# Optimization experiments

Measured on AMD Instinct MI355X. Metric: run time of the kernel, lower is better.

## Reference

```python
import jax, jax.numpy as jnp
import numpy as np

B, N = 512, 128
NFEAT, NHID, NHEADS, HID = 133, 60, 8, 300
FP_DIM, FP2, TASK = 1489, 512, 1
ALPHA = 0.2
NEG = -9e15


def _lin(k, fi, fo):
    s = 1.0 / np.sqrt(fi)
    return jax.random.uniform(k, (fi, fo), minval=-s, maxval=s, dtype=jnp.float32)


def _vec(k, fi, n):
    s = 1.0 / np.sqrt(fi)
    return jax.random.uniform(k, (n,), minval=-s, maxval=s, dtype=jnp.float32)


def setup_inputs() -> dict:
    key = jax.random.key(0)
    ks = jax.random.split(key, 24)
    x = jax.random.normal(ks[0], (B, N, NFEAT), dtype=jnp.float32)
    adj = jax.random.randint(ks[1], (B, N, N), 0, 2, dtype=jnp.int32)
    adj = jnp.maximum(adj, jnp.eye(N, dtype=jnp.int32)[None])  # ensure valid softmax rows
    fp = jax.random.uniform(ks[2], (B, FP_DIM), dtype=jnp.float32)
    # multi-head GAT params (W has no bias; attention vector a split into src/dst halves)
    sW = 1.0 / np.sqrt(NFEAT)
    W_heads = jax.random.uniform(ks[3], (NHEADS, NFEAT, NHID), minval=-sW, maxval=sW, dtype=jnp.float32)
    sa = 1.0 / np.sqrt(2 * NHID)
    a_src = jax.random.uniform(ks[4], (NHEADS, NHID), minval=-sa, maxval=sa, dtype=jnp.float32)
    a_dst = jax.random.uniform(ks[5], (NHEADS, NHID), minval=-sa, maxval=sa, dtype=jnp.float32)
    W_out = _lin(ks[6], NHEADS * NHID, HID)
    ao_src = _vec(ks[7], 2 * HID, HID)
    ao_dst = _vec(ks[8], 2 * HID, HID)
    fc1_w = _lin(ks[9], FP_DIM, FP2); fc1_b = _vec(ks[10], FP_DIM, FP2)
    fc2_w = _lin(ks[11], FP2, HID); fc2_b = _vec(ks[12], FP2, HID)
    fcg_w = _lin(ks[13], HID, HID); fcg_b = _vec(ks[14], HID, HID)
    fcf_w = _lin(ks[15], HID, HID); fcf_b = _vec(ks[16], HID, HID)
    ffn1_w = _lin(ks[17], 2 * HID, HID); ffn1_b = _vec(ks[18], 2 * HID, HID)
    ffn2_w = _lin(ks[19], HID, TASK); ffn2_b = _vec(ks[20], HID, TASK)
    return {"x": x, "adj": adj, "fp": fp, "W_heads": W_heads, "a_src": a_src,
            "a_dst": a_dst, "W_out": W_out, "ao_src": ao_src, "ao_dst": ao_dst,
            "fc1_w": fc1_w, "fc1_b": fc1_b, "fc2_w": fc2_w, "fc2_b": fc2_b,
            "fcg_w": fcg_w, "fcg_b": fcg_b, "fcf_w": fcf_w, "fcf_b": fcf_b,
            "ffn1_w": ffn1_w, "ffn1_b": ffn1_b, "ffn2_w": ffn2_w, "ffn2_b": ffn2_b}


def reference(x, adj, fp, W_heads, a_src, a_dst, W_out, ao_src, ao_dst,
              fc1_w, fc1_b, fc2_w, fc2_b, fcg_w, fcg_b, fcf_w, fcf_b,
              ffn1_w, ffn1_b, ffn2_w, ffn2_b):
    adjm = adj > 0  # [B,N,N]
    # --- multi-head GAT layer (dropout = identity in eval) ---
    Wh = jnp.einsum('bnf,hfo->bhno', x, W_heads)              # [B,H,N,nhid]
    s = jnp.einsum('bhno,ho->bhn', Wh, a_src)
    d = jnp.einsum('bhno,ho->bhn', Wh, a_dst)
    # e_ij = leakyrelu(a . [Wh_i ; Wh_j]) without materializing [N,N,2F]
    e = jax.nn.leaky_relu(s[:, :, :, None] + d[:, :, None, :], ALPHA)
    e = jnp.where(adjm[:, None], e, NEG)
    att = jax.nn.softmax(e, axis=-1)                          # softmax over neighbors j
    hp = jax.nn.elu(jnp.einsum('bhnm,bhmo->bhno', att, Wh))   # concat=True head output
    h = hp.transpose(0, 2, 1, 3).reshape(B, N, NHEADS * NHID)
    # --- output GAT layer (concat=False) ---
    Wo = h @ W_out                                            # [B,N,HID]
    eo = jax.nn.leaky_relu((Wo @ ao_src)[:, :, None] + (Wo @ ao_dst)[:, None, :], ALPHA)
    eo = jnp.where(adjm, eo, NEG)
    ho = jax.nn.softmax(eo, axis=-1) @ Wo
    ho = jax.nn.log_softmax(jax.nn.elu(ho), axis=-1)          # log_softmax over features (dim=1 in torch)
    gat = ho.mean(axis=1)                                     # sum over atoms / atom_size
    # --- FPN branch ---
    f = jax.nn.relu(fp @ fc1_w + fc1_b)
    f = f @ fc2_w + fc2_b
    # --- fusion (gat_scale = 0.5) ---
    g = jax.nn.relu(gat @ fcg_w + fcg_b)
    f = jax.nn.relu(f @ fcf_w + fcf_b)
    z = jnp.concatenate([g, f], axis=1)                       # [B, 2*HID]
    z = jax.nn.relu(z @ ffn1_w + ffn1_b)
    z = z @ ffn2_w + ffn2_b
    return jax.nn.sigmoid(z)                                  # is_classif, eval mode
```

## Files before the change

kernel.cpp:

```cpp
#include <hip/hip_runtime.h>
#include <hip/hip_bf16.h>
#include <math.h>
#include <stdint.h>

#define LRA 0.2f

typedef __attribute__((ext_vector_type(8))) short bf16x8;
typedef __attribute__((ext_vector_type(8))) unsigned short u16x8;
typedef __attribute__((ext_vector_type(4))) float f32x4;
typedef unsigned long long u64;

__device__ __forceinline__ unsigned short f2bf(float v) {
  union { __hip_bfloat16 b; unsigned short u; } c;
  c.b = __float2bfloat16(v);
  return c.u;
}
__device__ __forceinline__ float bf2f(unsigned short h) {
  union { float f; unsigned int u; } a; a.u = ((unsigned int)h) << 16;
  return a.f;
}
__device__ __forceinline__ float warp_sum(float v){
  #pragma unroll
  for (int s = 32; s; s >>= 1) v += __shfl_xor(v, s);
  return v;
}

__global__ __launch_bounds__(256) void k_mask(const int* __restrict__ adj, u64* __restrict__ mg){
  const int t = threadIdx.x, lane = t & 63, w = t >> 6, b = blockIdx.x;
  const int* adjb = adj + (size_t)b * 128 * 128;
  for (int i = w * 32; i < w * 32 + 32; ++i) {
    u64 b0 = __ballot(adjb[i * 128 + lane] > 0);
    u64 b1 = __ballot(adjb[i * 128 + 64 + lane] > 0);
    if (lane == 0) { mg[((size_t)b * 128 + i) * 2] = b0; mg[((size_t)b * 128 + i) * 2 + 1] = b1; }
  }
}

__global__ __launch_bounds__(64) void k_prep1(
    const float* __restrict__ Whw, unsigned short* __restrict__ BH, unsigned short* __restrict__ BL)
{
  const int kt = blockIdx.x, nt = blockIdx.y, l = threadIdx.x;
  const int n = nt * 16 + (l & 15), k0 = kt * 32 + (l >> 4) * 8;
  const int hd = n / 60, j = n - hd * 60;
  uint4 hv, lv;
  unsigned int* hp = (unsigned int*)&hv;
  unsigned int* lp = (unsigned int*)&lv;
  #pragma unroll
  for (int p = 0; p < 4; ++p) {
    unsigned short hh[2], ll[2];
    #pragma unroll
    for (int e = 0; e < 2; ++e) {
      const int k = k0 + p * 2 + e;
      const float v = (n < 480 && k < 133) ? Whw[((size_t)hd * 133 + k) * 60 + j] : 0.f;
      const unsigned short h = f2bf(v);
      hh[e] = h; ll[e] = f2bf(v - bf2f(h));
    }
    hp[p] = hh[0] | ((unsigned int)hh[1] << 16);
    lp[p] = ll[0] | ((unsigned int)ll[1] << 16);
  }
  const size_t off = (((size_t)(kt * 32 + nt)) * 64 + l) * 8;
  *(uint4*)&BH[off] = hv;
  *(uint4*)&BL[off] = lv;
}

__global__ __launch_bounds__(64) void k_prep2(
    const float* __restrict__ W, unsigned short* __restrict__ BH, unsigned short* __restrict__ BL)
{
  const int kt = blockIdx.x, nt = blockIdx.y, l = threadIdx.x;
  const int n = nt * 16 + (l & 15), k0 = kt * 32 + (l >> 4) * 8;
  uint4 hv, lv;
  unsigned int* hp = (unsigned int*)&hv;
  unsigned int* lp = (unsigned int*)&lv;
  #pragma unroll
  for (int p = 0; p < 4; ++p) {
    unsigned short hh[2], ll[2];
    #pragma unroll
    for (int e = 0; e < 2; ++e) {
      const int k = k0 + p * 2 + e;
      const float v = (n < 300 && k < 480) ? W[(size_t)k * 300 + n] : 0.f;
      const unsigned short h = f2bf(v);
      hh[e] = h; ll[e] = f2bf(v - bf2f(h));
    }
    hp[p] = hh[0] | ((unsigned int)hh[1] << 16);
    lp[p] = ll[0] | ((unsigned int)ll[1] << 16);
  }
  const size_t off = (((size_t)(kt * 20 + nt)) * 64 + l) * 8;
  *(uint4*)&BH[off] = hv;
  *(uint4*)&BL[off] = lv;
}

__global__ __launch_bounds__(512) void k_gemm1(
    const float* __restrict__ x,
    const unsigned short* __restrict__ BH, const unsigned short* __restrict__ BL,
    const float* __restrict__ asrc, const float* __restrict__ adst,
    unsigned int* __restrict__ buf1, float* __restrict__ s1g, float* __restrict__ d1g)
{
  __shared__ unsigned int Apk[64][32];
  __shared__ float asl[512], adl[512];
  __shared__ float sp0[8][64], sp1[8][64], dp0[8][64], dp1[8][64];
  const int t = threadIdx.x, lane = t & 63, w = t >> 6, r = lane & 15, g = lane >> 4;
  const int b = blockIdx.x >> 1, p = blockIdx.x & 1;
  const int row0 = p * 64;
  const float* xb = x + (size_t)b * 128 * 133;
  unsigned int* slab = buf1 + (size_t)b * 61440;

  asl[t] = (t < 480) ? asrc[t] : 0.f;
  adl[t] = (t < 480) ? adst[t] : 0.f;

  f32x4 acc[4][4];
  #pragma unroll
  for (int mt = 0; mt < 4; ++mt)
    #pragma unroll
    for (int ntl = 0; ntl < 4; ++ntl) acc[mt][ntl] = (f32x4){0.f,0.f,0.f,0.f};

  for (int kt = 0; kt < 5; ++kt) {
    {
      const int row_l = t >> 3, sl = t & 7;
      const int k0 = kt * 32 + sl * 4;
      uint4 pk;
      unsigned int* pp = (unsigned int*)&pk;
      #pragma unroll
      for (int e = 0; e < 4; ++e) {
        const int k = k0 + e;
        const float v = (k < 133) ? xb[(size_t)(row0 + row_l) * 133 + k] : 0.f;
        const unsigned short h = f2bf(v);
        pp[e] = ((unsigned int)h << 16) | f2bf(v - bf2f(h));
      }
      *(uint4*)&Apk[row_l][((sl ^ (row_l & 7)) << 2)] = pk;
    }
    bf16x8 bh[4], bl[4];
    #pragma unroll
    for (int ntl = 0; ntl < 4; ++ntl) {
      const int nt = w * 4 + ntl;
      const size_t off = (((size_t)(kt * 32 + nt)) * 64 + lane) * 8;
      bh[ntl] = *(const bf16x8*)&BH[off];
      bl[ntl] = *(const bf16x8*)&BL[off];
    }
    __syncthreads();
    #pragma unroll
    for (int mt = 0; mt < 4; ++mt) {
      const int row_l = mt * 16 + r, key = r & 7;
      const uint4 p0 = *(const uint4*)&Apk[row_l][(((2*g)   ^ key) << 2)];
      const uint4 p1 = *(const uint4*)&Apk[row_l][(((2*g+1) ^ key) << 2)];
      const unsigned int pw[8] = {p0.x,p0.y,p0.z,p0.w,p1.x,p1.y,p1.z,p1.w};
      bf16x8 ah, al;
      #pragma unroll
      for (int e = 0; e < 8; ++e) { ah[e] = (short)(pw[e] >> 16); al[e] = (short)(pw[e] & 0xffffu); }
      #pragma unroll
      for (int ntl = 0; ntl < 4; ++ntl) {
        acc[mt][ntl] = __builtin_amdgcn_mfma_f32_16x16x32_bf16(ah, bh[ntl], acc[mt][ntl], 0,0,0);
        acc[mt][ntl] = __builtin_amdgcn_mfma_f32_16x16x32_bf16(al, bh[ntl], acc[mt][ntl], 0,0,0);
        acc[mt][ntl] = __builtin_amdgcn_mfma_f32_16x16x32_bf16(ah, bl[ntl], acc[mt][ntl], 0,0,0);
      }
    }
    __syncthreads();
  }
  #pragma unroll
  for (int mt = 0; mt < 4; ++mt)
    #pragma unroll
    for (int ntl = 0; ntl < 4; ++ntl) {
      const int cc = (w * 4 + ntl) * 16 + r;
      if (cc < 480) {
        const int hd = cc / 60, cl = cc - hd * 60;
        uint4 pv;
        unsigned int* pp = (unsigned int*)&pv;
        #pragma unroll
        for (int q = 0; q < 4; ++q) {
          const float v = acc[mt][ntl][q];
          const unsigned short h = f2bf(v);
          pp[q] = ((unsigned int)h << 16) | f2bf(v - bf2f(h));
        }
        *(uint4*)&slab[(size_t)hd * 7680 + (size_t)cl * 128 + row0 + mt * 16 + (g << 2)] = pv;
      }
    }
  const int thr0 = 60 - 4 * w;
  #pragma unroll
  for (int mt = 0; mt < 4; ++mt) {
    #pragma unroll
    for (int q = 0; q < 4; ++q) {
      float s0 = 0.f, s1 = 0.f, d0 = 0.f, d1 = 0.f;
      #pragma unroll
      for (int ntl = 0; ntl < 4; ++ntl) {
        const int loc = ntl * 16 + r;
        const int cc = w * 64 + loc;
        const float a = acc[mt][ntl][q];
        const float as = asl[cc], ad = adl[cc];
        if (loc < thr0) { s0 += a * as; d0 += a * ad; }
        else            { s1 += a * as; d1 += a * ad; }
      }
      #pragma unroll
      for (int s = 1; s <= 8; s <<= 1) {
        s0 += __shfl_xor(s0, s); s1 += __shfl_xor(s1, s);
        d0 += __shfl_xor(d0, s); d1 += __shfl_xor(d1, s);
      }
      if (r == 0) {
        const int row_l = mt * 16 + g * 4 + q;
        sp0[w][row_l] = s0; sp1[w][row_l] = s1;
        dp0[w][row_l] = d0; dp1[w][row_l] = d1;
      }
    }
  }
  __syncthreads();
  {
    const int hd = t >> 6, row_l = t & 63;
    s1g[((size_t)b * 8 + hd) * 128 + row0 + row_l] = sp0[hd][row_l] + (hd > 0 ? sp1[hd-1][row_l] : 0.f);
    d1g[((size_t)b * 8 + hd) * 128 + row0 + row_l] = dp0[hd][row_l] + (hd > 0 ? dp1[hd-1][row_l] : 0.f);
  }
}

__device__ __forceinline__ float make_att_frags(
    const float si, const u64 ma, const u64 mb2, const float* darr,
    const int g, bf16x8* pah, bf16x8* pal)
{
  const unsigned int mby[4] = {
    (unsigned int)(ma  >> (g * 8)) & 0xffu,
    (unsigned int)(ma  >> (32 + g * 8)) & 0xffu,
    (unsigned int)(mb2 >> (g * 8)) & 0xffu,
    (unsigned int)(mb2 >> (32 + g * 8)) & 0xffu };
  float ev[4][8];
  float mx = -3e38f;
  #pragma unroll
  for (int kt = 0; kt < 4; ++kt)
    #pragma unroll
    for (int e = 0; e < 8; ++e) {
      const int j = ((kt & 1) * 32) + ((kt >> 1) * 64) + g * 8 + e;
      float v = si + darr[j];
      v = fmaxf(v, LRA * v);
      const float vv = (mby[((kt & 1) << 1) | (kt >> 1)] & (1u << e)) ? v : -3e38f;
      ev[kt][e] = vv;
      mx = fmaxf(mx, vv);
    }
  mx = fmaxf(mx, __shfl_xor(mx, 16));
  mx = fmaxf(mx, __shfl_xor(mx, 32));
  float sum = 0.f;
  #pragma unroll
  for (int kt = 0; kt < 4; ++kt)
    #pragma unroll
    for (int e = 0; e < 8; ++e) {
      const float p = (ev[kt][e] > -1e37f) ? __expf(ev[kt][e] - mx) : 0.f;
      ev[kt][e] = p;
      sum += p;
    }
  sum += __shfl_xor(sum, 16);
  sum += __shfl_xor(sum, 32);
  #pragma unroll
  for (int kt = 0; kt < 4; ++kt) {
    const int ks = ((kt & 1) << 1) | (kt >> 1);
    union { unsigned int u[4]; bf16x8 v; } hw, lw;
    #pragma unroll
    for (int p2 = 0; p2 < 4; ++p2) {
      const float p0 = ev[ks][2 * p2], p1 = ev[ks][2 * p2 + 1];
      const unsigned short h0 = f2bf(p0), h1 = f2bf(p1);
      hw.u[p2] = h0 | ((unsigned int)h1 << 16);
      lw.u[p2] = f2bf(p0 - bf2f(h0)) | ((unsigned int)f2bf(p1 - bf2f(h1)) << 16);
    }
    pah[kt] = hw.v;
    pal[kt] = lw.v;
  }
  return 1.f / sum;
}

__global__ __launch_bounds__(256) void k_att1(
    unsigned int* __restrict__ buf1, const u64* __restrict__ mg,
    const float* __restrict__ s1g, const float* __restrict__ d1g)
{
  __shared__ unsigned short Th[16][64][8], Tl[16][64][8];
  __shared__ float sarr[128], darr[128];
  __shared__ u64 mAr[128], mBr[128];
  const int t = threadIdx.x, lane = t & 63, w = t >> 6, r = lane & 15, g = lane >> 4;
  const int bid = blockIdx.x;
  const int lb = ((bid & 7) << 9) | (bid >> 3);
  const int b = lb >> 3, hd = lb & 7;
  const size_t sl = (size_t)b * 8 + hd;
  unsigned int* slab = buf1 + sl * 7680;

  if (t < 128) {
    sarr[t] = s1g[sl * 128 + t];
    darr[t] = d1g[sl * 128 + t];
    mAr[t] = mg[((size_t)b * 128 + t) * 2];
    mBr[t] = mg[((size_t)b * 128 + t) * 2 + 1];
  }
  #pragma unroll
  for (int ii = 0; ii < 4; ++ii) {
    const int idx = t + ii * 256;
    const int c = idx & 63, jg = idx >> 6;
    uint4 p0 = {0,0,0,0}, p1 = {0,0,0,0};
    if (c < 60) {
      const uint4* src = (const uint4*)&slab[(size_t)c * 128 + jg * 8];
      p0 = src[0]; p1 = src[1];
    }
    const unsigned int pw[8] = {p0.x,p0.y,p0.z,p0.w,p1.x,p1.y,p1.z,p1.w};
    u16x8 hv, lv;
    #pragma unroll
    for (int e = 0; e < 8; ++e) { hv[e] = (unsigned short)(pw[e] >> 16); lv[e] = (unsigned short)(pw[e] & 0xffffu); }
    const int tile = ((c >> 4) << 2) | (jg >> 2);
    const int li = ((jg & 3) << 4) | (c & 15);
    *(u16x8*)&Th[tile][li][0] = hv;
    *(u16x8*)&Tl[tile][li][0] = lv;
  }
  __syncthreads();
  bf16x8 pah[2][4], pal[2][4];
  float inv2[2];
  #pragma unroll
  for (int mt = 0; mt < 2; ++mt) {
    const int i = w * 32 + mt * 16 + r;
    inv2[mt] = make_att_frags(sarr[i], mAr[i], mBr[i], darr, g, pah[mt], pal[mt]);
  }
  f32x4 acc[2][4];
  #pragma unroll
  for (int mt = 0; mt < 2; ++mt)
    #pragma unroll
    for (int nt = 0; nt < 4; ++nt) acc[mt][nt] = (f32x4){0.f,0.f,0.f,0.f};
  #pragma unroll
  for (int kt = 0; kt < 4; ++kt)
    #pragma unroll
    for (int nt = 0; nt < 4; ++nt) {
      const bf16x8 bh = *(const bf16x8*)&Th[(nt << 2) | kt][lane][0];
      const bf16x8 bl = *(const bf16x8*)&Tl[(nt << 2) | kt][lane][0];
      #pragma unroll
      for (int mt = 0; mt < 2; ++mt) {
        acc[mt][nt] = __builtin_amdgcn_mfma_f32_16x16x32_bf16(pah[mt][kt], bh, acc[mt][nt], 0,0,0);
        acc[mt][nt] = __builtin_amdgcn_mfma_f32_16x16x32_bf16(pal[mt][kt], bh, acc[mt][nt], 0,0,0);
        acc[mt][nt] = __builtin_amdgcn_mfma_f32_16x16x32_bf16(pah[mt][kt], bl, acc[mt][nt], 0,0,0);
      }
    }
  #pragma unroll
  for (int mt = 0; mt < 2; ++mt) {
    float sc[4];
    #pragma unroll
    for (int q = 0; q < 4; ++q) sc[q] = __shfl(inv2[mt], g * 4 + q);
    #pragma unroll
    for (int nt = 0; nt < 4; ++nt) {
      const int cc = nt * 16 + r;
      if (cc < 60) {
        #pragma unroll
        for (int q = 0; q < 4; ++q) {
          const int row = w * 32 + mt * 16 + g * 4 + q;
          float v = acc[mt][nt][q] * sc[q];
          v = v > 0.f ? v : __expf(v) - 1.f;
          const unsigned short h = f2bf(v), l = f2bf(v - bf2f(h));
          slab[(size_t)row * 60 + cc] = ((unsigned int)h << 16) | l;
        }
      }
    }
  }
}

__global__ __launch_bounds__(256, 3) void k_gemm2(
    unsigned int* __restrict__ buf1,
    const unsigned short* __restrict__ BH, const unsigned short* __restrict__ BL,
    const float* __restrict__ aos, const float* __restrict__ aod,
    float* __restrict__ s2g, float* __restrict__ d2g)
{
  __shared__ unsigned int Apk[64][32];
  __shared__ float aosl[320], aodl[320];
  __shared__ float sred[4][64], dred[4][64];
  const int t = threadIdx.x, lane = t & 63, w = t >> 6, r = lane & 15, g = lane >> 4;
  const int b = blockIdx.x >> 1, p = blockIdx.x & 1;
  const int row0 = p * 64;
  unsigned int* slab = buf1 + (size_t)b * 61440;
  if (t < 320) { aosl[t] = t < 300 ? aos[t] : 0.f; aodl[t] = t < 300 ? aod[t] : 0.f; }

  f32x4 acc[4][5];
  #pragma unroll
  for (int mt = 0; mt < 4; ++mt)
    #pragma unroll
    for (int ntl = 0; ntl < 5; ++ntl) acc[mt][ntl] = (f32x4){0.f,0.f,0.f,0.f};

  for (int kt = 0; kt < 15; ++kt) {
    #pragma unroll
    for (int i = 0; i < 2; ++i) {
      const int idx = t + i * 256, row_l = idx >> 3, sl = idx & 7;
      const int k0 = kt * 32 + sl * 4;
      const int hd = k0 / 60, c = k0 - hd * 60;
      const uint4 v = *(const uint4*)&slab[(size_t)hd * 7680 + (size_t)(row0 + row_l) * 60 + c];
      *(uint4*)&Apk[row_l][((sl ^ (row_l & 7)) << 2)] = v;
    }
    bf16x8 bh[5], bl[5];
    #pragma unroll
    for (int ntl = 0; ntl < 5; ++ntl) {
      const int nt = w * 5 + ntl;
      const size_t off = (((size_t)(kt * 20 + nt)) * 64 + lane) * 8;
      bh[ntl] = *(const bf16x8*)&BH[off];
      bl[ntl] = *(const bf16x8*)&BL[off];
    }
    __syncthreads();
    #pragma unroll
    for (int mt = 0; mt < 4; ++mt) {
      const int row_l = mt * 16 + r, key = r & 7;
      const uint4 p0 = *(const uint4*)&Apk[row_l][(((2*g)   ^ key) << 2)];
      const uint4 p1 = *(const uint4*)&Apk[row_l][(((2*g+1) ^ key) << 2)];
      const unsigned int pw[8] = {p0.x,p0.y,p0.z,p0.w,p1.x,p1.y,p1.z,p1.w};
      bf16x8 ah, al;
      #pragma unroll
      for (int e = 0; e < 8; ++e) { ah[e] = (short)(pw[e] >> 16); al[e] = (short)(pw[e] & 0xffffu); }
      #pragma unroll
      for (int ntl = 0; ntl < 5; ++ntl) {
        acc[mt][ntl] = __builtin_amdgcn_mfma_f32_16x16x32_bf16(ah, bh[ntl], acc[mt][ntl], 0,0,0);
        acc[mt][ntl] = __builtin_amdgcn_mfma_f32_16x16x32_bf16(al, bh[ntl], acc[mt][ntl], 0,0,0);
        acc[mt][ntl] = __builtin_amdgcn_mfma_f32_16x16x32_bf16(ah, bl[ntl], acc[mt][ntl], 0,0,0);
      }
    }
    __syncthreads();
  }
  #pragma unroll
  for (int mt = 0; mt < 4; ++mt)
    #pragma unroll
    for (int ntl = 0; ntl < 5; ++ntl) {
      const int cc = w * 80 + ntl * 16 + r;
      if (cc < 300) {
        uint4 pv;
        unsigned int* pp = (unsigned int*)&pv;
        #pragma unroll
        for (int q = 0; q < 4; ++q) {
          const float v = acc[mt][ntl][q];
          const unsigned short h = f2bf(v);
          pp[q] = ((unsigned int)h << 16) | f2bf(v - bf2f(h));
        }
        *(uint4*)&slab[(size_t)cc * 128 + row0 + mt * 16 + (g << 2)] = pv;
      }
    }
  #pragma unroll
  for (int mt = 0; mt < 4; ++mt) {
    #pragma unroll
    for (int q = 0; q < 4; ++q) {
      float sv = 0.f, dv = 0.f;
      #pragma unroll
      for (int ntl = 0; ntl < 5; ++ntl) {
        const int cc = w * 80 + ntl * 16 + r;
        const float a = acc[mt][ntl][q];
        sv += a * aosl[cc]; dv += a * aodl[cc];
      }
      #pragma unroll
      for (int s = 1; s <= 8; s <<= 1) { sv += __shfl_xor(sv, s); dv += __shfl_xor(dv, s); }
      if (r == 0) {
        const int row_l = mt * 16 + g * 4 + q;
        sred[w][row_l] = sv; dred[w][row_l] = dv;
      }
    }
  }
  __syncthreads();
  if (t < 64) {
    s2g[(size_t)b * 128 + row0 + t] = sred[0][t] + sred[1][t] + sred[2][t] + sred[3][t];
    d2g[(size_t)b * 128 + row0 + t] = dred[0][t] + dred[1][t] + dred[2][t] + dred[3][t];
  }
}

__global__ __launch_bounds__(256) void k_att2(
    const unsigned int* __restrict__ buf1, const u64* __restrict__ mg,
    const float* __restrict__ s2g, const float* __restrict__ d2g,
    float* __restrict__ gat)
{
  __shared__ unsigned short Th[16][64][8], Tl[16][64][8];
  __shared__ float sarr[128], darr[128];
  __shared__ u64 mAr[128], mBr[128];
  __shared__ float colsum[304];
  __shared__ float srow[16];
  const int t = threadIdx.x, lane = t & 63, w = t >> 6, r = lane & 15, g = lane >> 4;
  const int b = blockIdx.x;
  const unsigned int* slab = buf1 + (size_t)b * 61440;

  if (t < 128) {
    sarr[t] = s2g[(size_t)b * 128 + t];
    darr[t] = d2g[(size_t)b * 128 + t];
    mAr[t] = mg[((size_t)b * 128 + t) * 2];
    mBr[t] = mg[((size_t)b * 128 + t) * 2 + 1];
  }
  for (int c = t; c < 304; c += 256) colsum[c] = 0.f;
  __syncthreads();
  bf16x8 pah[2][4], pal[2][4];
  float inv2[2];
  #pragma unroll
  for (int mt = 0; mt < 2; ++mt) {
    const int i = w * 32 + mt * 16 + r;
    inv2[mt] = make_att_frags(sarr[i], mAr[i], mBr[i], darr, g, pah[mt], pal[mt]);
  }
  float scq[2][4];
  #pragma unroll
  for (int mt = 0; mt < 2; ++mt)
    #pragma unroll
    for (int q = 0; q < 4; ++q) scq[mt][q] = __shfl(inv2[mt], g * 4 + q);

  float m8[2][4], l8[2][4];
  #pragma unroll
  for (int mt = 0; mt < 2; ++mt)
    #pragma unroll
    for (int q = 0; q < 4; ++q) { m8[mt][q] = -3e38f; l8[mt][q] = 0.f; }

  for (int ch = 0; ch < 5; ++ch) {
    #pragma unroll
    for (int ii = 0; ii < 4; ++ii) {
      const int idx = t + ii * 256;
      const int c = idx & 63, jg = idx >> 6;
      const int gc = ch * 64 + c;
      uint4 p0 = {0,0,0,0}, p1 = {0,0,0,0};
      if (gc < 300) {
        const uint4* src = (const uint4*)&slab[(size_t)gc * 128 + jg * 8];
        p0 = src[0]; p1 = src[1];
      }
      const unsigned int pw[8] = {p0.x,p0.y,p0.z,p0.w,p1.x,p1.y,p1.z,p1.w};
      u16x8 hv, lv;
      #pragma unroll
      for (int e = 0; e < 8; ++e) { hv[e] = (unsigned short)(pw[e] >> 16); lv[e] = (unsigned short)(pw[e] & 0xffffu); }
      const int tile = ((c >> 4) << 2) | (jg >> 2);
      const int li = ((jg & 3) << 4) | (c & 15);
      *(u16x8*)&Th[tile][li][0] = hv;
      *(u16x8*)&Tl[tile][li][0] = lv;
    }
    __syncthreads();
    f32x4 pacc[2][4];
    #pragma unroll
    for (int mt = 0; mt < 2; ++mt)
      #pragma unroll
      for (int nt = 0; nt < 4; ++nt) pacc[mt][nt] = (f32x4){0.f,0.f,0.f,0.f};
    #pragma unroll
    for (int kt = 0; kt < 4; ++kt)
      #pragma unroll
      for (int nt = 0; nt < 4; ++nt) {
        const bf16x8 bh = *(const bf16x8*)&Th[(nt << 2) | kt][lane][0];
        const bf16x8 bl = *(const bf16x8*)&Tl[(nt << 2) | kt][lane][0];
        #pragma unroll
        for (int mt = 0; mt < 2; ++mt) {
          pacc[mt][nt] = __builtin_amdgcn_mfma_f32_16x16x32_bf16(pah[mt][kt], bh, pacc[mt][nt], 0,0,0);
          pacc[mt][nt] = __builtin_amdgcn_mfma_f32_16x16x32_bf16(pal[mt][kt], bh, pacc[mt][nt], 0,0,0);
          pacc[mt][nt] = __builtin_amdgcn_mfma_f32_16x16x32_bf16(pah[mt][kt], bl, pacc[mt][nt], 0,0,0);
        }
      }
    float csA[4] = {0,0,0,0};
    #pragma unroll
    for (int mt = 0; mt < 2; ++mt) {
      float vq[4][4];
      #pragma unroll
      for (int nt = 0; nt < 4; ++nt) {
        const int cc = ch * 64 + nt * 16 + r;
        const bool cv = cc < 300;
        #pragma unroll
        for (int q = 0; q < 4; ++q) {
          float v = pacc[mt][nt][q] * scq[mt][q];
          v = v > 0.f ? v : __expf(v) - 1.f;
          vq[nt][q] = cv ? v : -3e38f;
          csA[nt] += cv ? v : 0.f;
        }
      }
      #pragma unroll
      for (int q = 0; q < 4; ++q) {
        float mx = fmaxf(fmaxf(vq[0][q], vq[1][q]), fmaxf(vq[2][q], vq[3][q]));
        mx = fmaxf(mx, __shfl_xor(mx, 1));
        mx = fmaxf(mx, __shfl_xor(mx, 2));
        mx = fmaxf(mx, __shfl_xor(mx, 4));
        mx = fmaxf(mx, __shfl_xor(mx, 8));
        const float nm = fmaxf(m8[mt][q], mx);
        float ps = __expf(vq[0][q]-nm) + __expf(vq[1][q]-nm) + __expf(vq[2][q]-nm) + __expf(vq[3][q]-nm);
        ps += __shfl_xor(ps, 1); ps += __shfl_xor(ps, 2);
        ps += __shfl_xor(ps, 4); ps += __shfl_xor(ps, 8);
        l8[mt][q] = l8[mt][q] * __expf(m8[mt][q] - nm) + ps;
        m8[mt][q] = nm;
      }
    }
    #pragma unroll
    for (int nt = 0; nt < 4; ++nt) {
      float cs = csA[nt];
      cs += __shfl_xor(cs, 16); cs += __shfl_xor(cs, 32);
      const int cc = ch * 64 + nt * 16 + r;
      if (g == 0 && cc < 300) atomicAdd(&colsum[cc], cs);
    }
    __syncthreads();
  }
  if (r == 0) {
    float sp = 0.f;
    #pragma unroll
    for (int mt = 0; mt < 2; ++mt)
      #pragma unroll
      for (int q = 0; q < 4; ++q) sp += m8[mt][q] + __logf(l8[mt][q]);
    srow[w * 4 + g] = sp;
  }
  __syncthreads();
  float S = 0.f;
  #pragma unroll
  for (int k = 0; k < 16; ++k) S += srow[k];
  for (int c = t; c < 300; c += 256)
    gat[(size_t)b * 300 + c] = (colsum[c] - S) * (1.f / 128.f);
}

__global__ __launch_bounds__(256) void k_gemm_sk(
    const float* __restrict__ A, const float* __restrict__ B,
    float* __restrict__ P, int M, int K, int N, int kpt)
{
  __shared__ unsigned short Ah[64][40], Al[64][40], Bh[64][40], Bl[64][40];
  const int t = threadIdx.x, lane = t & 63, w = t >> 6, r = lane & 15, g = lane >> 4;
  const int row0 = blockIdx.x * 64, col0 = blockIdx.y * 64;
// ... 30 lines not shown
      unsigned short h0 = f2bf(v0), h1 = f2bf(v1);
      *(unsigned int*)&Bh[n][kk] = h0 | ((unsigned int)h1 << 16);
      unsigned short l0 = f2bf(v0 - bf2f(h0)), l1 = f2bf(v1 - bf2f(h1));
      *(unsigned int*)&Bl[n][kk] = l0 | ((unsigned int)l1 << 16);
    }
    __syncthreads();
    const bf16x8 ah  = *(const bf16x8*)&Ah[w * 16 + r][g * 8];
    const bf16x8 al2 = *(const bf16x8*)&Al[w * 16 + r][g * 8];
    #pragma unroll
    for (int nt = 0; nt < 4; ++nt) {
      const bf16x8 bh = *(const bf16x8*)&Bh[nt * 16 + r][g * 8];
      const bf16x8 bl = *(const bf16x8*)&Bl[nt * 16 + r][g * 8];
      acc[nt] = __builtin_amdgcn_mfma_f32_16x16x32_bf16(ah,  bh, acc[nt], 0,0,0);
      acc[nt] = __builtin_amdgcn_mfma_f32_16x16x32_bf16(al2, bh, acc[nt], 0,0,0);
      acc[nt] = __builtin_amdgcn_mfma_f32_16x16x32_bf16(ah,  bl, acc[nt], 0,0,0);
    }
    __syncthreads();
  }
  float* Pout = P + (size_t)sk * M * N;
  #pragma unroll
  for (int nt = 0; nt < 4; ++nt) {
    const int cc = col0 + nt * 16 + r;
    if (cc < N) {
      #pragma unroll
      for (int q = 0; q < 4; ++q)
        Pout[(size_t)(row0 + w * 16 + g * 4 + q) * N + cc] = acc[nt][q];
    }
  }
}

__global__ __launch_bounds__(256) void k_reduce(
    const float* __restrict__ P, const float* __restrict__ bias,
    float* __restrict__ C, int M, int N, int ldc, int nsk, int act)
{
  const int idx = blockIdx.x * 256 + threadIdx.x;
  if (idx >= M * N) return;
  const int row = idx / N, col = idx - row * N;
  float s = bias[col];
  for (int k = 0; k < nsk; ++k) s += P[(size_t)k * M * N + idx];
  if (act) s = fmaxf(s, 0.f);
  C[(size_t)row * ldc + col] = s;
}

__global__ __launch_bounds__(512) void k_out(
    const float* __restrict__ z1, const float* __restrict__ w2,
    const float* __restrict__ b2, float* __restrict__ out)
{
  const int t = threadIdx.x, lane = t & 63, w = t >> 6;
  const int b = blockIdx.x * 8 + w;
  float p = 0.f;
  for (int k = lane; k < 300; k += 64) p += z1[(size_t)b * 300 + k] * w2[k];
  p = warp_sum(p);
  if (lane == 0) out[b] = 1.f / (1.f + __expf(-(p + b2[0])));
}

extern "C" void kernel_launch(void* const* d_in, const int* in_sizes, int n_in,
                              void* d_out, int out_size, void* d_ws, size_t ws_size,
                              hipStream_t stream)
{
  const float* x    = (const float*)d_in[0];
  const int*   adj  = (const int*)d_in[1];
  const float* fp   = (const float*)d_in[2];
  const float* Whw  = (const float*)d_in[3];
  const float* asrc = (const float*)d_in[4];
  const float* adst = (const float*)d_in[5];
  const float* Wout = (const float*)d_in[6];
  const float* aos  = (const float*)d_in[7];
  const float* aod  = (const float*)d_in[8];
  const float* fc1w = (const float*)d_in[9];
  const float* fc1b = (const float*)d_in[10];
  const float* fc2w = (const float*)d_in[11];
  const float* fc2b = (const float*)d_in[12];
  const float* fcgw = (const float*)d_in[13];
  const float* fcgb = (const float*)d_in[14];
  const float* fcfw = (const float*)d_in[15];
  const float* fcfb = (const float*)d_in[16];
  const float* f1w  = (const float*)d_in[17];
  const float* f1b  = (const float*)d_in[18];
  const float* f2w  = (const float*)d_in[19];
  const float* f2b  = (const float*)d_in[20];
  float* out = (float*)d_out;

  char* wsb = (char*)d_ws;
  unsigned int* buf1 = (unsigned int*)wsb;
  float* s1g = (float*)(wsb + 125829120);
  float* d1g = (float*)(wsb + 127926272);
  float* s2g = (float*)(wsb + 130023424);
  float* d2g = (float*)(wsb + 130285568);
  u64*   mgb = (u64*)  (wsb + 130547712);
  float* gatp = (float*)(wsb + 131596288);
  float* fpnp = (float*)(wsb + 132210688);
  float* f1buf = (float*)(wsb + 132825088);
  float* zb    = (float*)(wsb + 133873664);
  float* z1b   = (float*)(wsb + 135102464);
  float* P0 = (float*)(wsb + 135716864);
  float* P1 = (float*)(wsb + 142008320);
  float* P2 = (float*)(wsb + 144465920);
  float* P3 = (float*)(wsb + 145694720);
  float* P4 = (float*)(wsb + 146923520);
  unsigned short* Bf1H = (unsigned short*)(wsb + 149381120);
  unsigned short* Bf1L = (unsigned short*)(wsb + 149544960);
  unsigned short* Bf2H = (unsigned short*)(wsb + 149708800);
  unsigned short* Bf2L = (unsigned short*)(wsb + 150016000);

  k_prep1<<<dim3(5, 32), 64, 0, stream>>>(Whw, Bf1H, Bf1L);
  k_prep2<<<dim3(15, 20), 64, 0, stream>>>(Wout, Bf2H, Bf2L);
  k_mask <<<512, 256, 0, stream>>>(adj, mgb);
  k_gemm1<<<1024, 512, 0, stream>>>(x, Bf1H, Bf1L, asrc, adst, buf1, s1g, d1g);
  k_att1 <<<4096, 256, 0, stream>>>(buf1, mgb, s1g, d1g);
  k_gemm2<<<1024, 256, 0, stream>>>(buf1, Bf2H, Bf2L, aos, aod, s2g, d2g);
  k_att2 <<<512, 256, 0, stream>>>(buf1, mgb, s2g, d2g, gatp);
  k_gemm_sk<<<dim3(8,8,6), 256, 0, stream>>>(fp, fc1w, P0, 512, 1489, 512, 8);
  k_reduce<<<1024, 256, 0, stream>>>(P0, fc1b, f1buf, 512, 512, 512, 6, 1);
  k_gemm_sk<<<dim3(8,5,4), 256, 0, stream>>>(f1buf, fc2w, P1, 512, 512, 300, 4);
  k_reduce<<<600, 256, 0, stream>>>(P1, fc2b, fpnp, 512, 300, 300, 4, 0);
  k_gemm_sk<<<dim3(8,5,2), 256, 0, stream>>>(gatp, fcgw, P2, 512, 300, 300, 5);
  k_gemm_sk<<<dim3(8,5,2), 256, 0, stream>>>(fpnp, fcfw, P3, 512, 300, 300, 5);
  k_reduce<<<600, 256, 0, stream>>>(P2, fcgb, zb, 512, 300, 600, 2, 1);
  k_reduce<<<600, 256, 0, stream>>>(P3, fcfb, zb + 300, 512, 300, 600, 2, 1);
  k_gemm_sk<<<dim3(8,5,4), 256, 0, stream>>>(zb, f1w, P4, 512, 600, 300, 5);
  k_reduce<<<600, 256, 0, stream>>>(P4, f1b, z1b, 512, 300, 300, 4, 1);
  k_out<<<64, 512, 0, stream>>>(z1b, f2w, f2b, out);
}
```

Baseline: 376.6 us.

## Split attention score projections out of GEMM kernels into separate kernels

Removes the fused src/dst attention-score epilogues from k_gemm1 and k_gemm2 and computes them in new lightweight kernels (k_sd1, k_sd2) that reread the stored hi/lo bf16 outputs from global memory. k_gemm1 also halves its row tile from 64 to 32 rows, doubling the grid, and only half the threads stage A. The aim is to cut register and shared-memory pressure in the GEMMs and raise occupancy. In exchange it adds two kernel launches and an extra pass over the intermediate buffers. The scores are now computed from the split-rounded stored values rather than the fp32 accumulators.

After: 383.8 us. About the same (+1.9%).

```diff
diff --git a/kernel.cpp b/kernel.cpp
--- a/kernel.cpp
+++ b/kernel.cpp
@@ -91,29 +91,23 @@
 __global__ __launch_bounds__(512) void k_gemm1(
     const float* __restrict__ x,
     const unsigned short* __restrict__ BH, const unsigned short* __restrict__ BL,
-    const float* __restrict__ asrc, const float* __restrict__ adst,
-    unsigned int* __restrict__ buf1, float* __restrict__ s1g, float* __restrict__ d1g)
-{
-  __shared__ unsigned int Apk[64][32];
-  __shared__ float asl[512], adl[512];
-  __shared__ float sp0[8][64], sp1[8][64], dp0[8][64], dp1[8][64];
+    unsigned int* __restrict__ buf1)
+{
+  __shared__ unsigned int Apk[32][32];
   const int t = threadIdx.x, lane = t & 63, w = t >> 6, r = lane & 15, g = lane >> 4;
-  const int b = blockIdx.x >> 1, p = blockIdx.x & 1;
-  const int row0 = p * 64;
+  const int b = blockIdx.x >> 2, p = blockIdx.x & 3;
+  const int row0 = p * 32;
   const float* xb = x + (size_t)b * 128 * 133;
   unsigned int* slab = buf1 + (size_t)b * 61440;
 
-  asl[t] = (t < 480) ? asrc[t] : 0.f;
-  adl[t] = (t < 480) ? adst[t] : 0.f;
-
-  f32x4 acc[4][4];
-  #pragma unroll
-  for (int mt = 0; mt < 4; ++mt)
+  f32x4 acc[2][4];
+  #pragma unroll
+  for (int mt = 0; mt < 2; ++mt)
     #pragma unroll
     for (int ntl = 0; ntl < 4; ++ntl) acc[mt][ntl] = (f32x4){0.f,0.f,0.f,0.f};
 
   for (int kt = 0; kt < 5; ++kt) {
-    {
+    if (t < 256) {
       const int row_l = t >> 3, sl = t & 7;
       const int k0 = kt * 32 + sl * 4;
       uint4 pk;
@@ -137,7 +131,7 @@
     }
     __syncthreads();
     #pragma unroll
-    for (int mt = 0; mt < 4; ++mt) {
+    for (int mt = 0; mt < 2; ++mt) {
       const int row_l = mt * 16 + r, key = r & 7;
       const uint4 p0 = *(const uint4*)&Apk[row_l][(((2*g)   ^ key) << 2)];
       const uint4 p1 = *(const uint4*)&Apk[row_l][(((2*g+1) ^ key) << 2)];
@@ -155,7 +149,7 @@
     __syncthreads();
   }
   #pragma unroll
-  for (int mt = 0; mt < 4; ++mt)
+  for (int mt = 0; mt < 2; ++mt)
     #pragma unroll
     for (int ntl = 0; ntl < 4; ++ntl) {
       const int cc = (w * 4 + ntl) * 16 + r;
@@ -172,39 +166,45 @@
         *(uint4*)&slab[(size_t)hd * 7680 + (size_t)cl * 128 + row0 + mt * 16 + (g << 2)] = pv;
       }
     }
-  const int thr0 = 60 - 4 * w;
-  #pragma unroll
-  for (int mt = 0; mt < 4; ++mt) {
-    #pragma unroll
-    for (int q = 0; q < 4; ++q) {
-      float s0 = 0.f, s1 = 0.f, d0 = 0.f, d1 = 0.f;
-      #pragma unroll
-      for (int ntl = 0; ntl < 4; ++ntl) {
-        const int loc = ntl * 16 + r;
-        const int cc = w * 64 + loc;
-        const float a = acc[mt][ntl][q];
-        const float as = asl[cc], ad = adl[cc];
-        if (loc < thr0) { s0 += a * as; d0 += a * ad; }
-        else            { s1 += a * as; d1 += a * ad; }
-      }
-      #pragma unroll
-      for (int s = 1; s <= 8; s <<= 1) {
-        s0 += __shfl_xor(s0, s); s1 += __shfl_xor(s1, s);
-        d0 += __shfl_xor(d0, s); d1 += __shfl_xor(d1, s);
-      }
-      if (r == 0) {
-        const int row_l = mt * 16 + g * 4 + q;
-        sp0[w][row_l] = s0; sp1[w][row_l] = s1;
-        dp0[w][row_l] = d0; dp1[w][row_l] = d1;
-      }
-    }
-  }
-  __syncthreads();
-  {
-    const int hd = t >> 6, row_l = t & 63;
-    s1g[((size_t)b * 8 + hd) * 128 + row0 + row_l] = sp0[hd][row_l] + (hd > 0 ? sp1[hd-1][row_l] : 0.f);
-    d1g[((size_t)b * 8 + hd) * 128 + row0 + row_l] = dp0[hd][row_l] + (hd > 0 ? dp1[hd-1][row_l] : 0.f);
-  }
+}
+
+__global__ __launch_bounds__(64) void k_sd1(
+    const unsigned int* __restrict__ buf1, const float* __restrict__ asrc,
+    const float* __restrict__ adst, float* __restrict__ s1g, float* __restrict__ d1g)
+{
+  const int lane = threadIdx.x, sl = blockIdx.x, hd = sl & 7;
+  const unsigned int* slab = buf1 + (size_t)sl * 7680;
+  float s0 = 0.f, s1v = 0.f, d0 = 0.f, d1v = 0.f;
+  #pragma unroll 4
+  for (int c = 0; c < 60; ++c) {
+    const float ac = asrc[hd * 60 + c], dc = adst[hd * 60 + c];
+    const unsigned int p0 = slab[c * 128 + lane];
+    const unsigned int p1 = slab[c * 128 + 64 + lane];
+    const float v0 = bf2f((unsigned short)(p0 >> 16)) + bf2f((unsigned short)(p0 & 0xffffu));
+    const float v1 = bf2f((unsigned short)(p1 >> 16)) + bf2f((unsigned short)(p1 & 0xffffu));
+    s0 += v0 * ac; d0 += v0 * dc;
+    s1v += v1 * ac; d1v += v1 * dc;
+  }
+  s1g[(size_t)sl * 128 + lane] = s0;      d1g[(size_t)sl * 128 + lane] = d0;
+  s1g[(size_t)sl * 128 + 64 + lane] = s1v; d1g[(size_t)sl * 128 + 64 + lane] = d1v;
+}
+
+__global__ __launch_bounds__(128) void k_sd2(
+    const unsigned int* __restrict__ buf1, const float* __restrict__ aos,
+    const float* __restrict__ aod, float* __restrict__ s2g, float* __restrict__ d2g)
+{
+  const int j = threadIdx.x, b = blockIdx.x;
+  const unsigned int* slab = buf1 + (size_t)b * 61440;
+  float s = 0.f, d = 0.f;
+  #pragma unroll 4
+  for (int c = 0; c < 300; ++c) {
+    const float ac = aos[c], dc = aod[c];
+    const unsigned int pk = slab[(size_t)c * 128 + j];
+    const float v = bf2f((unsigned short)(pk >> 16)) + bf2f((unsigned short)(pk & 0xffffu));
+    s += v * ac; d += v * dc;
+  }
+  s2g[(size_t)b * 128 + j] = s;
+  d2g[(size_t)b * 128 + j] = d;
 }
 
 __device__ __forceinline__ float make_att_frags(
@@ -347,18 +347,13 @@
 
 __global__ __launch_bounds__(256, 3) void k_gemm2(
     unsigned int* __restrict__ buf1,
-    const unsigned short* __restrict__ BH, const unsigned short* __restrict__ BL,
-    const float* __restrict__ aos, const float* __restrict__ aod,
-    float* __restrict__ s2g, float* __restrict__ d2g)
+    const unsigned short* __restrict__ BH, const unsigned short* __restrict__ BL)
 {
   __shared__ unsigned int Apk[64][32];
-  __shared__ float aosl[320], aodl[320];
-  __shared__ float sred[4][64], dred[4][64];
   const int t = threadIdx.x, lane = t & 63, w = t >> 6, r = lane & 15, g = lane >> 4;
   const int b = blockIdx.x >> 1, p = blockIdx.x & 1;
   const int row0 = p * 64;
   unsigned int* slab = buf1 + (size_t)b * 61440;
-  if (t < 320) { aosl[t] = t < 300 ? aos[t] : 0.f; aodl[t] = t < 300 ? aod[t] : 0.f; }
 
   f32x4 acc[4][5];
   #pragma unroll
@@ -419,30 +414,6 @@
         *(uint4*)&slab[(size_t)cc * 128 + row0 + mt * 16 + (g << 2)] = pv;
       }
     }
-  #pragma unroll
-  for (int mt = 0; mt < 4; ++mt) {
-    #pragma unroll
-    for (int q = 0; q < 4; ++q) {
-      float sv = 0.f, dv = 0.f;
-      #pragma unroll
-      for (int ntl = 0; ntl < 5; ++ntl) {
-        const int cc = w * 80 + ntl * 16 + r;
-        const float a = acc[mt][ntl][q];
-        sv += a * aosl[cc]; dv += a * aodl[cc];
-      }
-      #pragma unroll
-      for (int s = 1; s <= 8; s <<= 1) { sv += __shfl_xor(sv, s); dv += __shfl_xor(dv, s); }
-      if (r == 0) {
-        const int row_l = mt * 16 + g * 4 + q;
-        sred[w][row_l] = sv; dred[w][row_l] = dv;
-      }
-    }
-  }
-  __syncthreads();
-  if (t < 64) {
-    s2g[(size_t)b * 128 + row0 + t] = sred[0][t] + sred[1][t] + sred[2][t] + sred[3][t];
-    d2g[(size_t)b * 128 + row0 + t] = dred[0][t] + dred[1][t] + dred[2][t] + dred[3][t];
-  }
 }
 
 __global__ __launch_bounds__(256) void k_att2(
@@ -725,9 +696,11 @@
   k_prep1<<<dim3(5, 32), 64, 0, stream>>>(Whw, Bf1H, Bf1L);
   k_prep2<<<dim3(15, 20), 64, 0, stream>>>(Wout, Bf2H, Bf2L);
   k_mask <<<512, 256, 0, stream>>>(adj, mgb);
-  k_gemm1<<<1024, 512, 0, stream>>>(x, Bf1H, Bf1L, asrc, adst, buf1, s1g, d1g);
+  k_gemm1<<<2048, 512, 0, stream>>>(x, Bf1H, Bf1L, buf1);
+  k_sd1  <<<4096, 64, 0, stream>>>(buf1, asrc, adst, s1g, d1g);
   k_att1 <<<4096, 256, 0, stream>>>(buf1, mgb, s1g, d1g);
-  k_gemm2<<<1024, 256, 0, stream>>>(buf1, Bf2H, Bf2L, aos, aod, s2g, d2g);
+  k_gemm2<<<1024, 256, 0, stream>>>(buf1, Bf2H, Bf2L);
+  k_sd2  <<<512, 128, 0, stream>>>(buf1, aos, aod, s2g, d2g);
   k_att2 <<<512, 256, 0, stream>>>(buf1, mgb, s2g, d2g, gatp);
   k_gemm_sk<<<dim3(8,8,6), 256, 0, stream>>>(fp, fc1w, P0, 512, 1489, 512, 8);
   k_reduce<<<1024, 256, 0, stream>>>(P0, fc1b, f1buf, 512, 512, 512, 6, 1);
```

## Split packed hi/lo bf16 intermediates into separate planes and halve gemm1 row tile

Applied to the files above, without the earlier changes.

Intermediate activations were stored as packed 32-bit words holding the bf16 hi and lo halves, and every consumer unpacked them with shifts and masks. They are now stored as two separate bf16 planes per batch, so MFMA A/B fragments load directly from shared memory with no unpack loops. The same change moves k_gemm1 to 32-row tiles across 2048 blocks, where half the threads sit idle while staging the A tile, and drops the XOR swizzle in favour of padded rows. The risks are extra global store and load instructions, possible LDS bank conflicts, and repeated B-fragment loads across twice as many gemm1 blocks.

Result: slower. 392.9 us (+4.3%).

```diff
diff --git a/kernel.cpp b/kernel.cpp
--- a/kernel.cpp
+++ b/kernel.cpp
@@ -92,40 +92,43 @@
     const float* __restrict__ x,
     const unsigned short* __restrict__ BH, const unsigned short* __restrict__ BL,
     const float* __restrict__ asrc, const float* __restrict__ adst,
-    unsigned int* __restrict__ buf1, float* __restrict__ s1g, float* __restrict__ d1g)
-{
-  __shared__ unsigned int Apk[64][32];
+    unsigned short* __restrict__ slabs, float* __restrict__ s1g, float* __restrict__ d1g)
+{
+  __shared__ unsigned short Ah[32][40], Al[32][40];
   __shared__ float asl[512], adl[512];
-  __shared__ float sp0[8][64], sp1[8][64], dp0[8][64], dp1[8][64];
+  __shared__ float sp0[8][32], sp1[8][32], dp0[8][32], dp1[8][32];
   const int t = threadIdx.x, lane = t & 63, w = t >> 6, r = lane & 15, g = lane >> 4;
-  const int b = blockIdx.x >> 1, p = blockIdx.x & 1;
-  const int row0 = p * 64;
+  const int b = blockIdx.x >> 2, p = blockIdx.x & 3;
+  const int row0 = p * 32;
   const float* xb = x + (size_t)b * 128 * 133;
-  unsigned int* slab = buf1 + (size_t)b * 61440;
+  unsigned short* WhH = slabs + (size_t)b * 122880;
+  unsigned short* WhL = WhH + 61440;
 
   asl[t] = (t < 480) ? asrc[t] : 0.f;
   adl[t] = (t < 480) ? adst[t] : 0.f;
 
-  f32x4 acc[4][4];
-  #pragma unroll
-  for (int mt = 0; mt < 4; ++mt)
+  f32x4 acc[2][4];
+  #pragma unroll
+  for (int mt = 0; mt < 2; ++mt)
     #pragma unroll
     for (int ntl = 0; ntl < 4; ++ntl) acc[mt][ntl] = (f32x4){0.f,0.f,0.f,0.f};
 
   for (int kt = 0; kt < 5; ++kt) {
-    {
+    if (t < 256) {
       const int row_l = t >> 3, sl = t & 7;
       const int k0 = kt * 32 + sl * 4;
-      uint4 pk;
-      unsigned int* pp = (unsigned int*)&pk;
+      unsigned short hh[4], ll[4];
       #pragma unroll
       for (int e = 0; e < 4; ++e) {
         const int k = k0 + e;
         const float v = (k < 133) ? xb[(size_t)(row0 + row_l) * 133 + k] : 0.f;
-        const unsigned short h = f2bf(v);
-        pp[e] = ((unsigned int)h << 16) | f2bf(v - bf2f(h));
-      }
-      *(uint4*)&Apk[row_l][((sl ^ (row_l & 7)) << 2)] = pk;
+        hh[e] = f2bf(v); ll[e] = f2bf(v - bf2f(hh[e]));
+      }
+      uint2 hv, lv;
+      hv.x = hh[0] | ((unsigned int)hh[1] << 16); hv.y = hh[2] | ((unsigned int)hh[3] << 16);
+      lv.x = ll[0] | ((unsigned int)ll[1] << 16); lv.y = ll[2] | ((unsigned int)ll[3] << 16);
+      *(uint2*)&Ah[row_l][sl * 4] = hv;
+      *(uint2*)&Al[row_l][sl * 4] = lv;
     }
     bf16x8 bh[4], bl[4];
     #pragma unroll
@@ -137,14 +140,10 @@
     }
     __syncthreads();
     #pragma unroll
-    for (int mt = 0; mt < 4; ++mt) {
-      const int row_l = mt * 16 + r, key = r & 7;
-      const uint4 p0 = *(const uint4*)&Apk[row_l][(((2*g)   ^ key) << 2)];
-      const uint4 p1 = *(const uint4*)&Apk[row_l][(((2*g+1) ^ key) << 2)];
-      const unsigned int pw[8] = {p0.x,p0.y,p0.z,p0.w,p1.x,p1.y,p1.z,p1.w};
-      bf16x8 ah, al;
-      #pragma unroll
-      for (int e = 0; e < 8; ++e) { ah[e] = (short)(pw[e] >> 16); al[e] = (short)(pw[e] & 0xffffu); }
+    for (int mt = 0; mt < 2; ++mt) {
+      const int row_l = mt * 16 + r;
+      const bf16x8 ah = *(const bf16x8*)&Ah[row_l][g * 8];
+      const bf16x8 al = *(const bf16x8*)&Al[row_l][g * 8];
       #pragma unroll
       for (int ntl = 0; ntl < 4; ++ntl) {
         acc[mt][ntl] = __builtin_amdgcn_mfma_f32_16x16x32_bf16(ah, bh[ntl], acc[mt][ntl], 0,0,0);
@@ -155,26 +154,29 @@
     __syncthreads();
   }
   #pragma unroll
-  for (int mt = 0; mt < 4; ++mt)
+  for (int mt = 0; mt < 2; ++mt)
     #pragma unroll
     for (int ntl = 0; ntl < 4; ++ntl) {
       const int cc = (w * 4 + ntl) * 16 + r;
       if (cc < 480) {
         const int hd = cc / 60, cl = cc - hd * 60;
-        uint4 pv;
-        unsigned int* pp = (unsigned int*)&pv;
+        unsigned short hh[4], ll[4];
         #pragma unroll
         for (int q = 0; q < 4; ++q) {
           const float v = acc[mt][ntl][q];
-          const unsigned short h = f2bf(v);
-          pp[q] = ((unsigned int)h << 16) | f2bf(v - bf2f(h));
+          hh[q] = f2bf(v); ll[q] = f2bf(v - bf2f(hh[q]));
         }
-        *(uint4*)&slab[(size_t)hd * 7680 + (size_t)cl * 128 + row0 + mt * 16 + (g << 2)] = pv;
+        uint2 hv, lv;
+        hv.x = hh[0] | ((unsigned int)hh[1] << 16); hv.y = hh[2] | ((unsigned int)hh[3] << 16);
+        lv.x = ll[0] | ((unsigned int)ll[1] << 16); lv.y = ll[2] | ((unsigned int)ll[3] << 16);
+        const size_t off = ((size_t)(hd * 60 + cl)) * 128 + row0 + mt * 16 + (g << 2);
+        *(uint2*)&WhH[off] = hv;
+        *(uint2*)&WhL[off] = lv;
       }
     }
   const int thr0 = 60 - 4 * w;
   #pragma unroll
-  for (int mt = 0; mt < 4; ++mt) {
+  for (int mt = 0; mt < 2; ++mt) {
     #pragma unroll
     for (int q = 0; q < 4; ++q) {
       float s0 = 0.f, s1 = 0.f, d0 = 0.f, d1 = 0.f;
@@ -200,8 +202,8 @@
     }
   }
   __syncthreads();
-  {
-    const int hd = t >> 6, row_l = t & 63;
+  if (t < 256) {
+    const int hd = t >> 5, row_l = t & 31;
     s1g[((size_t)b * 8 + hd) * 128 + row0 + row_l] = sp0[hd][row_l] + (hd > 0 ? sp1[hd-1][row_l] : 0.f);
     d1g[((size_t)b * 8 + hd) * 128 + row0 + row_l] = dp0[hd][row_l] + (hd > 0 ? dp1[hd-1][row_l] : 0.f);
   }
@@ -260,7 +262,7 @@
 }
 
 __global__ __launch_bounds__(256) void k_att1(
-    unsigned int* __restrict__ buf1, const u64* __restrict__ mg,
+    unsigned short* __restrict__ slabs, const u64* __restrict__ mg,
     const float* __restrict__ s1g, const float* __restrict__ d1g)
 {
   __shared__ unsigned short Th[16][64][8], Tl[16][64][8];
@@ -271,7 +273,8 @@
   const int lb = ((bid & 7) << 9) | (bid >> 3);
   const int b = lb >> 3, hd = lb & 7;
   const size_t sl = (size_t)b * 8 + hd;
-  unsigned int* slab = buf1 + sl * 7680;
+  unsigned short* WhHb = slabs + (size_t)b * 122880 + hd * 7680;
+  unsigned short* WhLb = WhHb + 61440;
 
   if (t < 128) {
     sarr[t] = s1g[sl * 128 + t];
@@ -283,19 +286,15 @@
   for (int ii = 0; ii < 4; ++ii) {
     const int idx = t + ii * 256;
     const int c = idx & 63, jg = idx >> 6;
-    uint4 p0 = {0,0,0,0}, p1 = {0,0,0,0};
+    uint4 hv = {0,0,0,0}, lv = {0,0,0,0};
     if (c < 60) {
-      const uint4* src = (const uint4*)&slab[(size_t)c * 128 + jg * 8];
-      p0 = src[0]; p1 = src[1];
-    }
-    const unsigned int pw[8] = {p0.x,p0.y,p0.z,p0.w,p1.x,p1.y,p1.z,p1.w};
-    u16x8 hv, lv;
-    #pragma unroll
-    for (int e = 0; e < 8; ++e) { hv[e] = (unsigned short)(pw[e] >> 16); lv[e] = (unsigned short)(pw[e] & 0xffffu); }
+      hv = *(const uint4*)&WhHb[(size_t)c * 128 + jg * 8];
+      lv = *(const uint4*)&WhLb[(size_t)c * 128 + jg * 8];
+    }
     const int tile = ((c >> 4) << 2) | (jg >> 2);
     const int li = ((jg & 3) << 4) | (c & 15);
-    *(u16x8*)&Th[tile][li][0] = hv;
-    *(u16x8*)&Tl[tile][li][0] = lv;
+    *(uint4*)&Th[tile][li][0] = hv;
+    *(uint4*)&Tl[tile][li][0] = lv;
   }
   __syncthreads();
   bf16x8 pah[2][4], pal[2][4];
@@ -337,8 +336,9 @@
           const int row = w * 32 + mt * 16 + g * 4 + q;
           float v = acc[mt][nt][q] * sc[q];
           v = v > 0.f ? v : __expf(v) - 1.f;
-          const unsigned short h = f2bf(v), l = f2bf(v - bf2f(h));
-          slab[(size_t)row * 60 + cc] = ((unsigned int)h << 16) | l;
+          const unsigned short h = f2bf(v);
+          WhHb[(size_t)row * 60 + cc] = h;
+          WhLb[(size_t)row * 60 + cc] = f2bf(v - bf2f(h));
         }
       }
     }
@@ -346,18 +346,19 @@
 }
 
 __global__ __launch_bounds__(256, 3) void k_gemm2(
-    unsigned int* __restrict__ buf1,
+    unsigned short* __restrict__ slabs,
     const unsigned short* __restrict__ BH, const unsigned short* __restrict__ BL,
     const float* __restrict__ aos, const float* __restrict__ aod,
     float* __restrict__ s2g, float* __restrict__ d2g)
 {
-  __shared__ unsigned int Apk[64][32];
+  __shared__ unsigned short Ah[64][40], Al[64][40];
   __shared__ float aosl[320], aodl[320];
   __shared__ float sred[4][64], dred[4][64];
   const int t = threadIdx.x, lane = t & 63, w = t >> 6, r = lane & 15, g = lane >> 4;
   const int b = blockIdx.x >> 1, p = blockIdx.x & 1;
   const int row0 = p * 64;
-  unsigned int* slab = buf1 + (size_t)b * 61440;
+  unsigned short* hH = slabs + (size_t)b * 122880;
+  unsigned short* hL = hH + 61440;
   if (t < 320) { aosl[t] = t < 300 ? aos[t] : 0.f; aodl[t] = t < 300 ? aod[t] : 0.f; }
 
   f32x4 acc[4][5];
@@ -372,8 +373,9 @@
       const int idx = t + i * 256, row_l = idx >> 3, sl = idx & 7;
       const int k0 = kt * 32 + sl * 4;
       const int hd = k0 / 60, c = k0 - hd * 60;
-      const uint4 v = *(const uint4*)&slab[(size_t)hd * 7680 + (size_t)(row0 + row_l) * 60 + c];
-      *(uint4*)&Apk[row_l][((sl ^ (row_l & 7)) << 2)] = v;
+      const size_t src = (size_t)hd * 7680 + (size_t)(row0 + row_l) * 60 + c;
+      *(uint2*)&Ah[row_l][sl * 4] = *(const uint2*)&hH[src];
+      *(uint2*)&Al[row_l][sl * 4] = *(const uint2*)&hL[src];
     }
     bf16x8 bh[5], bl[5];
     #pragma unroll
@@ -386,13 +388,9 @@
     __syncthreads();
     #pragma unroll
     for (int mt = 0; mt < 4; ++mt) {
-      const int row_l = mt * 16 + r, key = r & 7;
-      const uint4 p0 = *(const uint4*)&Apk[row_l][(((2*g)   ^ key) << 2)];
-      const uint4 p1 = *(const uint4*)&Apk[row_l][(((2*g+1) ^ key) << 2)];
-      const unsigned int pw[8] = {p0.x,p0.y,p0.z,p0.w,p1.x,p1.y,p1.z,p1.w};
-      bf16x8 ah, al;
-      #pragma unroll
-      for (int e = 0; e < 8; ++e) { ah[e] = (short)(pw[e] >> 16); al[e] = (short)(pw[e] & 0xffffu); }
+      const int row_l = mt * 16 + r;
+      const bf16x8 ah = *(const bf16x8*)&Ah[row_l][g * 8];
+      const bf16x8 al = *(const bf16x8*)&Al[row_l][g * 8];
       #pragma unroll
       for (int ntl = 0; ntl < 5; ++ntl) {
         acc[mt][ntl] = __builtin_amdgcn_mfma_f32_16x16x32_bf16(ah, bh[ntl], acc[mt][ntl], 0,0,0);
@@ -402,21 +400,26 @@
     }
     __syncthreads();
   }
+  unsigned short* WoH = hH;
+  unsigned short* WoL = hH + 38400;
   #pragma unroll
   for (int mt = 0; mt < 4; ++mt)
     #pragma unroll
     for (int ntl = 0; ntl < 5; ++ntl) {
       const int cc = w * 80 + ntl * 16 + r;
       if (cc < 300) {
-        uint4 pv;
-        unsigned int* pp = (unsigned int*)&pv;
+        unsigned short hh[4], ll[4];
         #pragma unroll
         for (int q = 0; q < 4; ++q) {
           const float v = acc[mt][ntl][q];
-          const unsigned short h = f2bf(v);
-          pp[q] = ((unsigned int)h << 16) | f2bf(v - bf2f(h));
+          hh[q] = f2bf(v); ll[q] = f2bf(v - bf2f(hh[q]));
         }
-        *(uint4*)&slab[(size_t)cc * 128 + row0 + mt * 16 + (g << 2)] = pv;
+        uint2 hv, lv;
+        hv.x = hh[0] | ((unsigned int)hh[1] << 16); hv.y = hh[2] | ((unsigned int)hh[3] << 16);
+        lv.x = ll[0] | ((unsigned int)ll[1] << 16); lv.y = ll[2] | ((unsigned int)ll[3] << 16);
+        const size_t off = (size_t)cc * 128 + row0 + mt * 16 + (g << 2);
+        *(uint2*)&WoH[off] = hv;
+        *(uint2*)&WoL[off] = lv;
       }
     }
   #pragma unroll
@@ -446,7 +449,7 @@
 }
 
 __global__ __launch_bounds__(256) void k_att2(
-    const unsigned int* __restrict__ buf1, const u64* __restrict__ mg,
+    const unsigned short* __restrict__ slabs, const u64* __restrict__ mg,
     const float* __restrict__ s2g, const float* __restrict__ d2g,
     float* __restrict__ gat)
 {
@@ -457,7 +460,8 @@
   __shared__ float srow[16];
   const int t = threadIdx.x, lane = t & 63, w = t >> 6, r = lane & 15, g = lane >> 4;
   const int b = blockIdx.x;
-  const unsigned int* slab = buf1 + (size_t)b * 61440;
+  const unsigned short* WoH = slabs + (size_t)b * 122880;
+  const unsigned short* WoL = WoH + 38400;
 
   if (t < 128) {
     sarr[t] = s2g[(size_t)b * 128 + t];
@@ -492,19 +496,15 @@
       const int idx = t + ii * 256;
       const int c = idx & 63, jg = idx >> 6;
       const int gc = ch * 64 + c;
-      uint4 p0 = {0,0,0,0}, p1 = {0,0,0,0};
+      uint4 hv = {0,0,0,0}, lv = {0,0,0,0};
       if (gc < 300) {
-        const uint4* src = (const uint4*)&slab[(size_t)gc * 128 + jg * 8];
-        p0 = src[0]; p1 = src[1];
-      }
-      const unsigned int pw[8] = {p0.x,p0.y,p0.z,p0.w,p1.x,p1.y,p1.z,p1.w};
-      u16x8 hv, lv;
-      #pragma unroll
-      for (int e = 0; e < 8; ++e) { hv[e] = (unsigned short)(pw[e] >> 16); lv[e] = (unsigned short)(pw[e] & 0xffffu); }
+        hv = *(const uint4*)&WoH[(size_t)gc * 128 + jg * 8];
+        lv = *(const uint4*)&WoL[(size_t)gc * 128 + jg * 8];
+      }
       const int tile = ((c >> 4) << 2) | (jg >> 2);
       const int li = ((jg & 3) << 4) | (c & 15);
-      *(u16x8*)&Th[tile][li][0] = hv;
-      *(u16x8*)&Tl[tile][li][0] = lv;
+      *(uint4*)&Th[tile][li][0] = hv;
+      *(uint4*)&Tl[tile][li][0] = lv;
     }
     __syncthreads();
     f32x4 pacc[2][4];
@@ -701,7 +701,7 @@
   float* out = (float*)d_out;
 
   char* wsb = (char*)d_ws;
-  unsigned int* buf1 = (unsigned int*)wsb;
+  unsigned short* slabs = (unsigned short*)wsb;
   float* s1g = (float*)(wsb + 125829120);
   float* d1g = (float*)(wsb + 127926272);
   float* s2g = (float*)(wsb + 130023424);
@@ -725,10 +725,10 @@
   k_prep1<<<dim3(5, 32), 64, 0, stream>>>(Whw, Bf1H, Bf1L);
   k_prep2<<<dim3(15, 20), 64, 0, stream>>>(Wout, Bf2H, Bf2L);
   k_mask <<<512, 256, 0, stream>>>(adj, mgb);
-  k_gemm1<<<1024, 512, 0, stream>>>(x, Bf1H, Bf1L, asrc, adst, buf1, s1g, d1g);
-  k_att1 <<<4096, 256, 0, stream>>>(buf1, mgb, s1g, d1g);
-  k_gemm2<<<1024, 256, 0, stream>>>(buf1, Bf2H, Bf2L, aos, aod, s2g, d2g);
-  k_att2 <<<512, 256, 0, stream>>>(buf1, mgb, s2g, d2g, gatp);
+  k_gemm1<<<2048, 512, 0, stream>>>(x, Bf1H, Bf1L, asrc, adst, slabs, s1g, d1g);
+  k_att1 <<<4096, 256, 0, stream>>>(slabs, mgb, s1g, d1g);
+  k_gemm2<<<1024, 256, 0, stream>>>(slabs, Bf2H, Bf2L, aos, aod, s2g, d2g);
+  k_att2 <<<512, 256, 0, stream>>>(slabs, mgb, s2g, d2g, gatp);
   k_gemm_sk<<<dim3(8,8,6), 256, 0, stream>>>(fp, fc1w, P0, 512, 1489, 512, 8);
   k_reduce<<<1024, 256, 0, stream>>>(P0, fc1b, f1buf, 512, 512, 512, 6, 1);
   k_gemm_sk<<<dim3(8,5,4), 256, 0, stream>>>(f1buf, fc2w, P1, 512, 512, 300, 4);
```
